# Optimization experiments

Measured on AMD Instinct MI355X. Metric: run time of the kernel, lower is better.

Reference implementation:

```python
import jax, jax.numpy as jnp
import numpy as np

B, N, NPOINT, K = 16, 4096, 1024, 8
CIN, COUT = 128, 256
RADIUS = 0.2
BN_EPS = 1e-5


def fps(pts, npoint):
    # pts: [B, N, 3] -> indices [B, npoint], farthest point sampling starting at index 0
    b, n, _ = pts.shape

    def body(carry, _):
        dists, last = carry  # dists [B,N], last [B]
        cur = jnp.take_along_axis(pts, last[:, None, None], axis=1)  # [B,1,3]
        d = jnp.sum((pts - cur) ** 2, axis=-1)  # [B,N]
        dists = jnp.minimum(dists, d)
        nxt = jnp.argmax(dists, axis=-1).astype(jnp.int32)
        return (dists, nxt), last

    init = (jnp.full((b, n), jnp.finfo(pts.dtype).max, pts.dtype),
            jnp.zeros((b,), jnp.int32))
    _, idxs = jax.lax.scan(body, init, None, length=npoint)  # [npoint, B]
    return idxs.T  # [B, npoint]


def ball_query(new_xyz, pts, radius, k):
    # new_xyz [B,S,3], pts [B,N,3] -> idx [B,S,k] (pad with first in-ball index, pointnet2 semantics)
    n = pts.shape[1]
    d2 = jnp.sum((new_xyz[:, :, None, :] - pts[:, None, :, :]) ** 2, axis=-1)  # [B,S,N]
    cand = jnp.where(d2 <= radius * radius, jnp.arange(n, dtype=jnp.int32), n)
    idx = jnp.sort(cand, axis=-1)[..., :k]  # first k in-ball indices (center always in-ball)
    idx = jnp.where(idx == n, idx[..., :1], idx)
    return idx


def setup_inputs() -> dict:
    key = jax.random.key(0)
    ks = jax.random.split(key, 8)
    xyz = jax.random.uniform(ks[0], (B, 3, N), dtype=jnp.float32)
    feat = jax.random.normal(ks[1], (B, CIN, N), dtype=jnp.float32)
    conv_w = jax.random.normal(ks[2], (COUT, CIN), dtype=jnp.float32) * (1.0 / np.sqrt(CIN))
    conv_b = jax.random.normal(ks[3], (COUT,), dtype=jnp.float32) * 0.01
    bn_gamma = jax.random.uniform(ks[4], (COUT,), dtype=jnp.float32, minval=0.5, maxval=1.5)
    bn_beta = jax.random.normal(ks[5], (COUT,), dtype=jnp.float32) * 0.1
    bn_mean = jax.random.normal(ks[6], (COUT,), dtype=jnp.float32) * 0.1
    bn_var = jax.random.uniform(ks[7], (COUT,), dtype=jnp.float32, minval=0.5, maxval=1.5)
    return {"xyz": xyz, "feat": feat, "conv_w": conv_w, "conv_b": conv_b,
            "bn_gamma": bn_gamma, "bn_beta": bn_beta, "bn_mean": bn_mean, "bn_var": bn_var}


def reference(xyz, feat, conv_w, conv_b, bn_gamma, bn_beta, bn_mean, bn_var):
    pts = jnp.transpose(xyz, (0, 2, 1))   # [B,N,3]
    fts = jnp.transpose(feat, (0, 2, 1))  # [B,N,F]

    fps_idx = fps(pts, NPOINT)                                        # [B,S]
    new_xyz = jnp.take_along_axis(pts, fps_idx[..., None], axis=1)    # [B,S,3]

    idx = ball_query(new_xyz, pts, RADIUS, K)                          # [B,S,K]
    grouped = jax.vmap(lambda f, i: f[i])(fts, idx)                    # [B,S,K,F]

    # shared pointwise Conv1d (kernel 1) + BatchNorm (inference stats) + ReLU
    x = jnp.einsum('bskf,of->bsko', grouped, conv_w) + conv_b          # [B,S,K,COUT]
    x = bn_gamma * (x - bn_mean) / jnp.sqrt(bn_var + BN_EPS) + bn_beta
    x = jax.nn.relu(x)
    new_feat = jnp.max(x, axis=2)                                      # [B,S,COUT]
    return new_xyz, new_feat
```

## Files before the change

### kernel.cpp

```cpp
#include <hip/hip_runtime.h>
#include <hip/hip_bf16.h>
#include <stdint.h>

#define Bn   16
#define Nn   4096
#define Sn   1024
#define Kn   8
#define CINn 128
#define COUTn 256

typedef __attribute__((ext_vector_type(8))) short bf16x8;
typedef __attribute__((ext_vector_type(4))) float f32x4;
typedef unsigned short ushort;
typedef __attribute__((ext_vector_type(8))) unsigned short ushort8;

static __device__ __forceinline__ float sqdist(float ax, float ay, float az,
                                               float bx, float by, float bz) {
    float dx = __fsub_rn(ax, bx);
    float dy = __fsub_rn(ay, by);
    float dz = __fsub_rn(az, bz);
    return __fadd_rn(__fadd_rn(__fmul_rn(dx, dx), __fmul_rn(dy, dy)), __fmul_rn(dz, dz));
}

static __device__ __forceinline__ unsigned long long u64max(unsigned long long a,
                                                            unsigned long long b) {
    return a > b ? a : b;
}

static __device__ __forceinline__ ushort f2bf(float f) {
    unsigned x = __float_as_uint(f);
    unsigned r = x + 0x7FFFu + ((x >> 16) & 1u);
    return (ushort)(r >> 16);
}

template <int CTRL>
static __device__ __forceinline__ void dpp_max_level(int& lo, int& hi) {
    int olo = __builtin_amdgcn_update_dpp(lo, lo, CTRL, 0xF, 0xF, false);
    int ohi = __builtin_amdgcn_update_dpp(hi, hi, CTRL, 0xF, 0xF, false);
    unsigned long long o = ((unsigned long long)(unsigned)ohi << 32) | (unsigned)olo;
    unsigned long long k = ((unsigned long long)(unsigned)hi << 32) | (unsigned)lo;
    if (o > k) { lo = olo; hi = ohi; }
}

static __device__ __forceinline__ unsigned long long wave_max_u64(unsigned long long key) {
    int lo = (int)(unsigned)(key & 0xFFFFFFFFull);
    int hi = (int)(unsigned)(key >> 32);
    dpp_max_level<0x111>(lo, hi);
    dpp_max_level<0x112>(lo, hi);
    dpp_max_level<0x114>(lo, hi);
    dpp_max_level<0x118>(lo, hi);
    dpp_max_level<0x142>(lo, hi);
    dpp_max_level<0x143>(lo, hi);
    unsigned flo = (unsigned)__builtin_amdgcn_readlane(lo, 63);
    unsigned fhi = (unsigned)__builtin_amdgcn_readlane(hi, 63);
    return ((unsigned long long)fhi << 32) | flo;
}

__global__ __launch_bounds__(256) void k_fps(const float* __restrict__ xyz,
                                             float* __restrict__ out_xyz) {
    __shared__ __align__(16) float xs[Nn], ys[Nn], zs[Nn];
    __shared__ __align__(16) unsigned long long gbuf[2][4];
    const int b = blockIdx.x;
    const int tid = threadIdx.x;
    const int wid = tid >> 6, lane = tid & 63;
    const float* base = xyz + (size_t)b * 3 * Nn;
    for (int i = tid; i < Nn; i += 256) {
        xs[i] = base[i];
        ys[i] = base[Nn + i];
        zs[i] = base[2 * Nn + i];
    }
    __syncthreads();
    float px[16], py[16], pz[16], dist[16];
#pragma unroll
    for (int j = 0; j < 16; ++j) {
        int p = tid + j * 256;
        px[j] = xs[p]; py[j] = ys[p]; pz[j] = zs[p];
        dist[j] = 3.402823466e+38f;
    }
    int last = 0;
    if (tid == 0) {
        out_xyz[(size_t)(b * Sn) * 3 + 0] = xs[0];
        out_xyz[(size_t)(b * Sn) * 3 + 1] = ys[0];
        out_xyz[(size_t)(b * Sn) * 3 + 2] = zs[0];
    }
    for (int s = 1; s < Sn; ++s) {
        const float cx = xs[last], cy = ys[last], cz = zs[last];
        float mv = -1.0f; int mi = 0;
#pragma unroll
        for (int j = 0; j < 16; ++j) {
            float d = sqdist(px[j], py[j], pz[j], cx, cy, cz);
            float nd = fminf(dist[j], d);
            dist[j] = nd;
            if (nd > mv) { mv = nd; mi = tid + j * 256; }
        }
        unsigned long long key =
            ((unsigned long long)__float_as_uint(mv) << 32) | (unsigned)(Nn - 1 - mi);
        key = wave_max_u64(key);
        if (lane == 0) gbuf[s & 1][wid] = key;
        __syncthreads();
        const ulonglong2 g0 = *(const ulonglong2*)&gbuf[s & 1][0];
        const ulonglong2 g1 = *(const ulonglong2*)&gbuf[s & 1][2];
        key = u64max(u64max(g0.x, g0.y), u64max(g1.x, g1.y));
        const int nl = Nn - 1 - (int)(unsigned)(key & 0xFFFFFFFFull);
        if (tid == 0) {
            out_xyz[(size_t)(b * Sn + s) * 3 + 0] = xs[nl];
            out_xyz[(size_t)(b * Sn + s) * 3 + 1] = ys[nl];
            out_xyz[(size_t)(b * Sn + s) * 3 + 2] = zs[nl];
        }
        last = nl;
    }
}

static __device__ __forceinline__ void wave_ball(const float* __restrict__ base,
                                                 float cx, float cy, float cz,
                                                 int lane, int* bslot) {
    int cnt = 0;
    int idx0 = -1;
    for (int chunk = 0; chunk < Nn / 64; ++chunk) {
        const int p = chunk * 64 + lane;
        const float d2 = sqdist(base[p], base[Nn + p], base[2 * Nn + p], cx, cy, cz);
        const bool in = (d2 <= 0.04f);
        const unsigned long long m = __ballot(in);
        if (m != 0ull) {
            if (idx0 < 0) idx0 = chunk * 64 + __builtin_ctzll(m);
            const int rank = cnt + __popcll(m & ((1ull << lane) - 1ull));
            if (in && rank < Kn)
                bslot[rank] = p;
            cnt += __popcll(m);
            if (cnt >= Kn) break;
        }
    }
    if (lane < Kn && lane >= cnt)
        bslot[lane] = idx0;
}

__global__ __launch_bounds__(512) void k_feat(const float* __restrict__ xyz,
                                              const float* __restrict__ out_xyz,
                                              const float* __restrict__ feat,
                                              const float* __restrict__ conv_w,
                                              const float* __restrict__ conv_b,
                                              const float* __restrict__ bn_g,
                                              const float* __restrict__ bn_b,
                                              const float* __restrict__ bn_m,
                                              const float* __restrict__ bn_v,
                                              float* __restrict__ out_feat) {
    __shared__ __align__(16) ushort A_lds[64][136];
    __shared__ __align__(16) ushort Wc[COUTn][40];
    __shared__ int bidx[8][Kn];
    const int tid = threadIdx.x;
    const int wave = tid >> 6, lane = tid & 63;
    const int b  = blockIdx.x & 15;
    const int c0 = (blockIdx.x >> 4) * 8;
    const int bs = b * Sn + c0 + wave;

    const float* base = xyz + (size_t)b * 3 * Nn;
    const float cx = out_xyz[(size_t)bs * 3 + 0];
    const float cy = out_xyz[(size_t)bs * 3 + 1];
    const float cz = out_xyz[(size_t)bs * 3 + 2];
    wave_ball(base, cx, cy, cz, lane, &bidx[wave][0]);
    __syncthreads();

    const float* fb = feat + (size_t)b * CINn * Nn;
    {
        const int r = tid >> 3, fo = tid & 7;
        const int pt = bidx[r >> 3][r & 7];
        ushort us[16];
#pragma unroll
        for (int i = 0; i < 16; ++i)
            us[i] = f2bf(fb[(size_t)(fo * 16 + i) * Nn + pt]);
        *(ushort8*)&A_lds[r][fo * 16]     = *(const ushort8*)&us[0];
        *(ushort8*)&A_lds[r][fo * 16 + 8] = *(const ushort8*)&us[8];
    }

    const int wo = tid >> 1, wfh = tid & 1;
    float4 stgW[4];
    {
        const float4* src = (const float4*)(conv_w + (size_t)wo * CINn + wfh * 16);
#pragma unroll
        for (int i = 0; i < 4; ++i) stgW[i] = src[i];
    }

    const int mt = wave & 3;
    const int obase = (wave >> 2) * 128;
    f32x4 acc[8];
#pragma unroll
    for (int t = 0; t < 8; ++t) acc[t] = (f32x4){0.f, 0.f, 0.f, 0.f};

    const int arow = mt * 16 + (lane & 15);
    const int kgrp = (lane >> 4) * 8;

#pragma unroll
    for (int ks = 0; ks < 4; ++ks) {
        {
            ushort us[16];
#pragma unroll
            for (int i = 0; i < 4; ++i) {
                us[i * 4 + 0] = f2bf(stgW[i].x);
                us[i * 4 + 1] = f2bf(stgW[i].y);
                us[i * 4 + 2] = f2bf(stgW[i].z);
                us[i * 4 + 3] = f2bf(stgW[i].w);
            }
            *(ushort8*)&Wc[wo][wfh * 16]     = *(const ushort8*)&us[0];
            *(ushort8*)&Wc[wo][wfh * 16 + 8] = *(const ushort8*)&us[8];
        }
        __syncthreads();
        if (ks < 3) {
            const float4* src = (const float4*)(conv_w + (size_t)wo * CINn +
                                                (ks + 1) * 32 + wfh * 16);
#pragma unroll
            for (int i = 0; i < 4; ++i) stgW[i] = src[i];
        }
        const bf16x8 a = *(const bf16x8*)&A_lds[arow][ks * 32 + kgrp];
#pragma unroll
        for (int t = 0; t < 8; ++t) {
            const int o = obase + t * 16 + (lane & 15);
            const bf16x8 bb = *(const bf16x8*)&Wc[o][kgrp];
            acc[t] = __builtin_amdgcn_mfma_f32_16x16x32_bf16(a, bb, acc[t], 0, 0, 0);
        }
        __syncthreads();
    }

    const int half = lane >> 4;
#pragma unroll
    for (int t = 0; t < 8; ++t) {
        const int o = obase + t * 16 + (lane & 15);
        const float bias = conv_b[o];
        const float g = bn_g[o], be = bn_b[o], mn = bn_m[o], vr = bn_v[o];
        const float inv = sqrtf(vr + 1e-5f);
        float m4 = -3.402823466e+38f;
#pragma unroll
        for (int i = 0; i < 4; ++i) {
            float z = acc[t][i] + bias;
            float y = g * (z - mn) / inv + be;
            y = fmaxf(y, 0.0f);
            m4 = fmaxf(m4, y);
        }
        const float mo = __shfl_xor(m4, 16);
        const float mx = fmaxf(m4, mo);
        if (half == 0)
            out_feat[(size_t)(b * Sn + c0 + mt * 2) * COUTn + o] = mx;
        else if (half == 2)
            out_feat[(size_t)(b * Sn + c0 + mt * 2 + 1) * COUTn + o] = mx;
    }
}

extern "C" void kernel_launch(void* const* d_in, const int* in_sizes, int n_in,
                              void* d_out, int out_size, void* d_ws, size_t ws_size,
                              hipStream_t stream) {
    const float* xyz    = (const float*)d_in[0];
    const float* feat   = (const float*)d_in[1];
    const float* conv_w = (const float*)d_in[2];
    const float* conv_b = (const float*)d_in[3];
    const float* bn_g   = (const float*)d_in[4];
    const float* bn_b   = (const float*)d_in[5];
    const float* bn_m   = (const float*)d_in[6];
    const float* bn_v   = (const float*)d_in[7];

    float* out_xyz  = (float*)d_out;
    float* out_feat = out_xyz + (size_t)Bn * Sn * 3;

    k_fps <<<dim3(Bn),           dim3(256), 0, stream>>>(xyz, out_xyz);
    k_feat<<<dim3(Bn * Sn / 8),  dim3(512), 0, stream>>>(xyz, out_xyz, feat,
                                                         conv_w, conv_b,
                                                         bn_g, bn_b, bn_m, bn_v,
                                                         out_feat);
}
```

Baseline: 707.3 us.

## Pack FPS distance math into float2 and broadcast winner coords via shared memory

The FPS loop now uses two-wide float vectors so the compiler can emit packed FP32 ops (v_pk_*) for the distance update. The winning lane of each wave writes the candidate point's coordinates next to its key, so after the barrier every thread selects the new centroid coordinates directly. This removes the dependent LDS lookup of xs/ys/zs by index at the start of each iteration. Each thread now does a speculative LDS read of its local argmax coordinates every step, and fp contract is disabled to keep rounding identical.

```diff
diff --git a/kernel.cpp b/kernel.cpp
--- a/kernel.cpp
+++ b/kernel.cpp
@@ -11,6 +11,7 @@
 
 typedef __attribute__((ext_vector_type(8))) short bf16x8;
 typedef __attribute__((ext_vector_type(4))) float f32x4;
+typedef __attribute__((ext_vector_type(2))) float f32x2;
 typedef unsigned short ushort;
 typedef __attribute__((ext_vector_type(8))) unsigned short ushort8;
 
@@ -58,11 +59,13 @@
 
 __global__ __launch_bounds__(256) void k_fps(const float* __restrict__ xyz,
                                              float* __restrict__ out_xyz) {
+#pragma clang fp contract(off)
     __shared__ __align__(16) float xs[Nn], ys[Nn], zs[Nn];
-    __shared__ __align__(16) unsigned long long gbuf[2][4];
+    __shared__ __align__(16) unsigned long long kbuf[2][4];
+    __shared__ __align__(16) float4 cbuf[2][4];
     const int b = blockIdx.x;
     const int tid = threadIdx.x;
-    const int wid = tid >> 6, lane = tid & 63;
+    const int wid = tid >> 6;
     const float* base = xyz + (size_t)b * 3 * Nn;
     for (int i = tid; i < Nn; i += 256) {
         xs[i] = base[i];
@@ -70,44 +73,67 @@
         zs[i] = base[2 * Nn + i];
     }
     __syncthreads();
-    float px[16], py[16], pz[16], dist[16];
-#pragma unroll
-    for (int j = 0; j < 16; ++j) {
-        int p = tid + j * 256;
-        px[j] = xs[p]; py[j] = ys[p]; pz[j] = zs[p];
-        dist[j] = 3.402823466e+38f;
-    }
-    int last = 0;
+    f32x2 px[8], py[8], pz[8], dist[8];
+#pragma unroll
+    for (int j = 0; j < 8; ++j) {
+        const int p0 = tid + (2 * j) * 256, p1 = p0 + 256;
+        px[j] = (f32x2){xs[p0], xs[p1]};
+        py[j] = (f32x2){ys[p0], ys[p1]};
+        pz[j] = (f32x2){zs[p0], zs[p1]};
+        dist[j] = (f32x2){3.402823466e+38f, 3.402823466e+38f};
+    }
+    float cx = xs[0], cy = ys[0], cz = zs[0];
     if (tid == 0) {
-        out_xyz[(size_t)(b * Sn) * 3 + 0] = xs[0];
-        out_xyz[(size_t)(b * Sn) * 3 + 1] = ys[0];
-        out_xyz[(size_t)(b * Sn) * 3 + 2] = zs[0];
+        out_xyz[(size_t)(b * Sn) * 3 + 0] = cx;
+        out_xyz[(size_t)(b * Sn) * 3 + 1] = cy;
+        out_xyz[(size_t)(b * Sn) * 3 + 2] = cz;
     }
     for (int s = 1; s < Sn; ++s) {
-        const float cx = xs[last], cy = ys[last], cz = zs[last];
+        const f32x2 cx2 = (f32x2){cx, cx};
+        const f32x2 cy2 = (f32x2){cy, cy};
+        const f32x2 cz2 = (f32x2){cz, cz};
         float mv = -1.0f; int mi = 0;
 #pragma unroll
-        for (int j = 0; j < 16; ++j) {
-            float d = sqdist(px[j], py[j], pz[j], cx, cy, cz);
-            float nd = fminf(dist[j], d);
-            dist[j] = nd;
-            if (nd > mv) { mv = nd; mi = tid + j * 256; }
-        }
-        unsigned long long key =
+        for (int j = 0; j < 8; ++j) {
+            f32x2 dx = px[j] - cx2;
+            f32x2 dy = py[j] - cy2;
+            f32x2 dz = pz[j] - cz2;
+            f32x2 xx = dx * dx, yy = dy * dy, zz = dz * dz;
+            f32x2 ss = (xx + yy) + zz;
+            const float n0 = fminf(dist[j].x, ss.x);
+            const float n1 = fminf(dist[j].y, ss.y);
+            dist[j].x = n0; dist[j].y = n1;
+            if (n0 > mv) { mv = n0; mi = tid + (2 * j) * 256; }
+            if (n1 > mv) { mv = n1; mi = tid + (2 * j + 1) * 256; }
+        }
+        const float wx = xs[mi], wy = ys[mi], wz = zs[mi];
+        const unsigned long long mykey =
             ((unsigned long long)__float_as_uint(mv) << 32) | (unsigned)(Nn - 1 - mi);
-        key = wave_max_u64(key);
-        if (lane == 0) gbuf[s & 1][wid] = key;
+        const unsigned long long wkey = wave_max_u64(mykey);
+        if (mykey == wkey) {
+            kbuf[s & 1][wid] = wkey;
+            cbuf[s & 1][wid] = make_float4(wx, wy, wz, 0.0f);
+        }
         __syncthreads();
-        const ulonglong2 g0 = *(const ulonglong2*)&gbuf[s & 1][0];
-        const ulonglong2 g1 = *(const ulonglong2*)&gbuf[s & 1][2];
-        key = u64max(u64max(g0.x, g0.y), u64max(g1.x, g1.y));
-        const int nl = Nn - 1 - (int)(unsigned)(key & 0xFFFFFFFFull);
+        const ulonglong2 kv0 = *(const ulonglong2*)&kbuf[s & 1][0];
+        const ulonglong2 kv1 = *(const ulonglong2*)&kbuf[s & 1][2];
+        const float4 c0 = cbuf[s & 1][0];
+        const float4 c1 = cbuf[s & 1][1];
+        const float4 c2 = cbuf[s & 1][2];
+        const float4 c3 = cbuf[s & 1][3];
+        const bool b01 = kv0.y > kv0.x;
+        const bool b23 = kv1.y > kv1.x;
+        const unsigned long long k01 = b01 ? kv0.y : kv0.x;
+        const unsigned long long k23 = b23 ? kv1.y : kv1.x;
+        const float4 ca = b01 ? c1 : c0;
+        const float4 cb = b23 ? c3 : c2;
+        const float4 cw = (k23 > k01) ? cb : ca;
+        cx = cw.x; cy = cw.y; cz = cw.z;
         if (tid == 0) {
-            out_xyz[(size_t)(b * Sn + s) * 3 + 0] = xs[nl];
-            out_xyz[(size_t)(b * Sn + s) * 3 + 1] = ys[nl];
-            out_xyz[(size_t)(b * Sn + s) * 3 + 2] = zs[nl];
-        }
-        last = nl;
+            out_xyz[(size_t)(b * Sn + s) * 3 + 0] = cx;
+            out_xyz[(size_t)(b * Sn + s) * 3 + 1] = cy;
+            out_xyz[(size_t)(b * Sn + s) * 3 + 2] = cz;
+        }
     }
 }
 
```

Result: no change. 709.4 us (+0.3%).

## Fuse FPS and grouping/conv into one persistent kernel with progress flags

Applied to the files above, without the earlier changes.

Merges the FPS kernel and the ball-query/conv kernel into a single persistent launch. 16 blocks run FPS and publish a per-batch progress counter every 64 samples. The remaining blocks spin on that counter and process feature tiles as soon as their centroids are ready. This overlaps the serial FPS phase with the grouping and MFMA work, which previously ran only after FPS finished. The cost is a spin-wait protocol built on relaxed atomics, and the whole scheme relies on all 240 blocks being co-resident on the GPU.

```diff
diff --git a/kernel.cpp b/kernel.cpp
--- a/kernel.cpp
+++ b/kernel.cpp
@@ -9,10 +9,18 @@
 #define CINn 128
 #define COUTn 256
 
+#define NFPS 16
+#define NBLK 240
+
 typedef __attribute__((ext_vector_type(8))) short bf16x8;
 typedef __attribute__((ext_vector_type(4))) float f32x4;
 typedef unsigned short ushort;
 typedef __attribute__((ext_vector_type(8))) unsigned short ushort8;
+
+#define ATOM_ST_F32(p, v) __hip_atomic_store((p), (v), __ATOMIC_RELAXED, __HIP_MEMORY_SCOPE_AGENT)
+#define ATOM_LD_F32(p)    __hip_atomic_load((p), __ATOMIC_RELAXED, __HIP_MEMORY_SCOPE_AGENT)
+#define ATOM_ST_I32(p, v) __hip_atomic_store((p), (v), __ATOMIC_RELAXED, __HIP_MEMORY_SCOPE_AGENT)
+#define ATOM_LD_I32(p)    __hip_atomic_load((p), __ATOMIC_RELAXED, __HIP_MEMORY_SCOPE_AGENT)
 
 static __device__ __forceinline__ float sqdist(float ax, float ay, float az,
                                                float bx, float by, float bz) {
@@ -54,61 +62,6 @@
     unsigned flo = (unsigned)__builtin_amdgcn_readlane(lo, 63);
     unsigned fhi = (unsigned)__builtin_amdgcn_readlane(hi, 63);
     return ((unsigned long long)fhi << 32) | flo;
-}
-
-__global__ __launch_bounds__(256) void k_fps(const float* __restrict__ xyz,
-                                             float* __restrict__ out_xyz) {
-    __shared__ __align__(16) float xs[Nn], ys[Nn], zs[Nn];
-    __shared__ __align__(16) unsigned long long gbuf[2][4];
-    const int b = blockIdx.x;
-    const int tid = threadIdx.x;
-    const int wid = tid >> 6, lane = tid & 63;
-    const float* base = xyz + (size_t)b * 3 * Nn;
-    for (int i = tid; i < Nn; i += 256) {
-        xs[i] = base[i];
-        ys[i] = base[Nn + i];
-        zs[i] = base[2 * Nn + i];
-    }
-    __syncthreads();
-    float px[16], py[16], pz[16], dist[16];
-#pragma unroll
-    for (int j = 0; j < 16; ++j) {
-        int p = tid + j * 256;
-        px[j] = xs[p]; py[j] = ys[p]; pz[j] = zs[p];
-        dist[j] = 3.402823466e+38f;
-    }
-    int last = 0;
-    if (tid == 0) {
-        out_xyz[(size_t)(b * Sn) * 3 + 0] = xs[0];
-        out_xyz[(size_t)(b * Sn) * 3 + 1] = ys[0];
-        out_xyz[(size_t)(b * Sn) * 3 + 2] = zs[0];
-    }
-    for (int s = 1; s < Sn; ++s) {
-        const float cx = xs[last], cy = ys[last], cz = zs[last];
-        float mv = -1.0f; int mi = 0;
-#pragma unroll
-        for (int j = 0; j < 16; ++j) {
-            float d = sqdist(px[j], py[j], pz[j], cx, cy, cz);
-            float nd = fminf(dist[j], d);
-            dist[j] = nd;
-            if (nd > mv) { mv = nd; mi = tid + j * 256; }
-        }
-        unsigned long long key =
-            ((unsigned long long)__float_as_uint(mv) << 32) | (unsigned)(Nn - 1 - mi);
-        key = wave_max_u64(key);
-        if (lane == 0) gbuf[s & 1][wid] = key;
-        __syncthreads();
-        const ulonglong2 g0 = *(const ulonglong2*)&gbuf[s & 1][0];
-        const ulonglong2 g1 = *(const ulonglong2*)&gbuf[s & 1][2];
-        key = u64max(u64max(g0.x, g0.y), u64max(g1.x, g1.y));
-        const int nl = Nn - 1 - (int)(unsigned)(key & 0xFFFFFFFFull);
-        if (tid == 0) {
-            out_xyz[(size_t)(b * Sn + s) * 3 + 0] = xs[nl];
-            out_xyz[(size_t)(b * Sn + s) * 3 + 1] = ys[nl];
-            out_xyz[(size_t)(b * Sn + s) * 3 + 2] = zs[nl];
-        }
-        last = nl;
-    }
 }
 
 static __device__ __forceinline__ void wave_ball(const float* __restrict__ base,
@@ -134,113 +87,194 @@
         bslot[lane] = idx0;
 }
 
-__global__ __launch_bounds__(512) void k_feat(const float* __restrict__ xyz,
-                                              const float* __restrict__ out_xyz,
-                                              const float* __restrict__ feat,
-                                              const float* __restrict__ conv_w,
-                                              const float* __restrict__ conv_b,
-                                              const float* __restrict__ bn_g,
-                                              const float* __restrict__ bn_b,
-                                              const float* __restrict__ bn_m,
-                                              const float* __restrict__ bn_v,
-                                              float* __restrict__ out_feat) {
-    __shared__ __align__(16) ushort A_lds[64][136];
-    __shared__ __align__(16) ushort Wc[COUTn][40];
-    __shared__ int bidx[8][Kn];
+__global__ __launch_bounds__(512, 2) void k_fused(
+        const float* __restrict__ xyz,
+        const float* __restrict__ feat,
+        const float* __restrict__ conv_w,
+        const float* __restrict__ conv_b,
+        const float* __restrict__ bn_g,
+        const float* __restrict__ bn_b,
+        const float* __restrict__ bn_m,
+        const float* __restrict__ bn_v,
+        float* __restrict__ out_xyz,
+        float* __restrict__ out_feat,
+        int* __restrict__ progress) {
+    __shared__ __align__(16) char shm[86016];
     const int tid = threadIdx.x;
+    const int bid = blockIdx.x;
+
+    if (bid < NFPS) {
+        const int b = bid;
+        if (tid >= 256) {
+            for (int s = 0; s < Sn; ++s) __syncthreads();
+            return;
+        }
+        float* xs = (float*)shm;
+        float* ys = xs + Nn;
+        float* zs = ys + Nn;
+        unsigned long long (*gbuf)[4] =
+            (unsigned long long(*)[4])(shm + 3 * Nn * sizeof(float));
+        const int wid = tid >> 6, lane = tid & 63;
+        const float* base = xyz + (size_t)b * 3 * Nn;
+        for (int i = tid; i < Nn; i += 256) {
+            xs[i] = base[i];
+            ys[i] = base[Nn + i];
+            zs[i] = base[2 * Nn + i];
+        }
+        __syncthreads();
+        float px[16], py[16], pz[16], dist[16];
+#pragma unroll
+        for (int j = 0; j < 16; ++j) {
+            int p = tid + j * 256;
+            px[j] = xs[p]; py[j] = ys[p]; pz[j] = zs[p];
+            dist[j] = 3.402823466e+38f;
+        }
+        int last = 0;
+        if (tid == 0) {
+            ATOM_ST_F32(&out_xyz[(size_t)(b * Sn) * 3 + 0], xs[0]);
+            ATOM_ST_F32(&out_xyz[(size_t)(b * Sn) * 3 + 1], ys[0]);
+            ATOM_ST_F32(&out_xyz[(size_t)(b * Sn) * 3 + 2], zs[0]);
+        }
+        for (int s = 1; s < Sn; ++s) {
+            const float cx = xs[last], cy = ys[last], cz = zs[last];
+            float mv = -1.0f; int mi = 0;
+#pragma unroll
+            for (int j = 0; j < 16; ++j) {
+                float d = sqdist(px[j], py[j], pz[j], cx, cy, cz);
+                float nd = fminf(dist[j], d);
+                dist[j] = nd;
+                if (nd > mv) { mv = nd; mi = tid + j * 256; }
+            }
+            unsigned long long key =
+                ((unsigned long long)__float_as_uint(mv) << 32) |
+                (unsigned)(Nn - 1 - mi);
+            key = wave_max_u64(key);
+            if (lane == 0) gbuf[s & 1][wid] = key;
+            __syncthreads();
+            const ulonglong2 g0 = *(const ulonglong2*)&gbuf[s & 1][0];
+            const ulonglong2 g1 = *(const ulonglong2*)&gbuf[s & 1][2];
+            key = u64max(u64max(g0.x, g0.y), u64max(g1.x, g1.y));
+            const int nl = Nn - 1 - (int)(unsigned)(key & 0xFFFFFFFFull);
+            if (tid == 0) {
+                ATOM_ST_F32(&out_xyz[(size_t)(b * Sn + s) * 3 + 0], xs[nl]);
+                ATOM_ST_F32(&out_xyz[(size_t)(b * Sn + s) * 3 + 1], ys[nl]);
+                ATOM_ST_F32(&out_xyz[(size_t)(b * Sn + s) * 3 + 2], zs[nl]);
+                if ((s & 63) == 63) {
+                    asm volatile("s_waitcnt vmcnt(0)" ::: "memory");
+                    ATOM_ST_I32(progress + b, s + 1);
+                }
+            }
+            last = nl;
+        }
+        return;
+    }
+
+    ushort (*A_lds)[136] = (ushort(*)[136])shm;
+    ushort (*Wc)[40]     = (ushort(*)[40])(shm + 17408);
+    int (*bidx)[Kn]      = (int(*)[Kn])(shm + 17408 + 20480);
     const int wave = tid >> 6, lane = tid & 63;
-    const int b  = blockIdx.x & 15;
-    const int c0 = (blockIdx.x >> 4) * 8;
-    const int bs = b * Sn + c0 + wave;
-
-    const float* base = xyz + (size_t)b * 3 * Nn;
-    const float cx = out_xyz[(size_t)bs * 3 + 0];
-    const float cy = out_xyz[(size_t)bs * 3 + 1];
-    const float cz = out_xyz[(size_t)bs * 3 + 2];
-    wave_ball(base, cx, cy, cz, lane, &bidx[wave][0]);
-    __syncthreads();
-
-    const float* fb = feat + (size_t)b * CINn * Nn;
-    {
-        const int r = tid >> 3, fo = tid & 7;
-        const int pt = bidx[r >> 3][r & 7];
-        ushort us[16];
-#pragma unroll
-        for (int i = 0; i < 16; ++i)
-            us[i] = f2bf(fb[(size_t)(fo * 16 + i) * Nn + pt]);
-        *(ushort8*)&A_lds[r][fo * 16]     = *(const ushort8*)&us[0];
-        *(ushort8*)&A_lds[r][fo * 16 + 8] = *(const ushort8*)&us[8];
-    }
-
-    const int wo = tid >> 1, wfh = tid & 1;
-    float4 stgW[4];
-    {
-        const float4* src = (const float4*)(conv_w + (size_t)wo * CINn + wfh * 16);
-#pragma unroll
-        for (int i = 0; i < 4; ++i) stgW[i] = src[i];
-    }
-
-    const int mt = wave & 3;
-    const int obase = (wave >> 2) * 128;
-    f32x4 acc[8];
-#pragma unroll
-    for (int t = 0; t < 8; ++t) acc[t] = (f32x4){0.f, 0.f, 0.f, 0.f};
-
-    const int arow = mt * 16 + (lane & 15);
-    const int kgrp = (lane >> 4) * 8;
-
-#pragma unroll
-    for (int ks = 0; ks < 4; ++ks) {
+
+    for (int t = bid - NFPS; t < Bn * Sn / 8; t += NBLK - NFPS) {
+        const int b  = t & 15;
+        const int c0 = (t >> 4) * 8;
+        const int bs = b * Sn + c0 + wave;
+
+        if (tid == 0) {
+            while (ATOM_LD_I32(progress + b) < c0 + 8)
+                __builtin_amdgcn_s_sleep(8);
+        }
+        __syncthreads();
+
+        const float cx = ATOM_LD_F32(&out_xyz[(size_t)bs * 3 + 0]);
+        const float cy = ATOM_LD_F32(&out_xyz[(size_t)bs * 3 + 1]);
+        const float cz = ATOM_LD_F32(&out_xyz[(size_t)bs * 3 + 2]);
+
+        const float* base = xyz + (size_t)b * 3 * Nn;
+        wave_ball(base, cx, cy, cz, lane, &bidx[wave][0]);
+        __syncthreads();
+
+        const float* fb = feat + (size_t)b * CINn * Nn;
         {
+            const int r = tid >> 3, fo = tid & 7;
+            const int pt = bidx[r >> 3][r & 7];
             ushort us[16];
 #pragma unroll
+            for (int i = 0; i < 16; ++i)
+                us[i] = f2bf(fb[(size_t)(fo * 16 + i) * Nn + pt]);
+            *(ushort8*)&A_lds[r][fo * 16]     = *(const ushort8*)&us[0];
+            *(ushort8*)&A_lds[r][fo * 16 + 8] = *(const ushort8*)&us[8];
+        }
+
+        const int wo = tid >> 1, wfh = tid & 1;
+        float4 stgW[4];
+        {
+            const float4* src = (const float4*)(conv_w + (size_t)wo * CINn + wfh * 16);
+#pragma unroll
+            for (int i = 0; i < 4; ++i) stgW[i] = src[i];
+        }
+
+        const int mt = wave & 3;
+        const int obase = (wave >> 2) * 128;
+        f32x4 acc[8];
+#pragma unroll
+        for (int tt = 0; tt < 8; ++tt) acc[tt] = (f32x4){0.f, 0.f, 0.f, 0.f};
+
+        const int arow = mt * 16 + (lane & 15);
+        const int kgrp = (lane >> 4) * 8;
+
+#pragma unroll
+        for (int ks = 0; ks < 4; ++ks) {
+            {
+                ushort us[16];
+#pragma unroll
+                for (int i = 0; i < 4; ++i) {
+                    us[i * 4 + 0] = f2bf(stgW[i].x);
+                    us[i * 4 + 1] = f2bf(stgW[i].y);
+                    us[i * 4 + 2] = f2bf(stgW[i].z);
+                    us[i * 4 + 3] = f2bf(stgW[i].w);
+                }
+                *(ushort8*)&Wc[wo][wfh * 16]     = *(const ushort8*)&us[0];
+                *(ushort8*)&Wc[wo][wfh * 16 + 8] = *(const ushort8*)&us[8];
+            }
+            __syncthreads();
+            if (ks < 3) {
+                const float4* src = (const float4*)(conv_w + (size_t)wo * CINn +
+                                                    (ks + 1) * 32 + wfh * 16);
+#pragma unroll
+                for (int i = 0; i < 4; ++i) stgW[i] = src[i];
+            }
+            const bf16x8 a = *(const bf16x8*)&A_lds[arow][ks * 32 + kgrp];
+#pragma unroll
+            for (int tt = 0; tt < 8; ++tt) {
+                const int o = obase + tt * 16 + (lane & 15);
+                const bf16x8 bb = *(const bf16x8*)&Wc[o][kgrp];
+                acc[tt] = __builtin_amdgcn_mfma_f32_16x16x32_bf16(a, bb, acc[tt], 0, 0, 0);
+            }
+            __syncthreads();
+        }
+
+        const int half = lane >> 4;
+#pragma unroll
+        for (int tt = 0; tt < 8; ++tt) {
+            const int o = obase + tt * 16 + (lane & 15);
+            const float bias = conv_b[o];
+            const float g = bn_g[o], be = bn_b[o], mn = bn_m[o], vr = bn_v[o];
+            const float inv = sqrtf(vr + 1e-5f);
+            float m4 = -3.402823466e+38f;
+#pragma unroll
             for (int i = 0; i < 4; ++i) {
-                us[i * 4 + 0] = f2bf(stgW[i].x);
-                us[i * 4 + 1] = f2bf(stgW[i].y);
-                us[i * 4 + 2] = f2bf(stgW[i].z);
-                us[i * 4 + 3] = f2bf(stgW[i].w);
-            }
-            *(ushort8*)&Wc[wo][wfh * 16]     = *(const ushort8*)&us[0];
-            *(ushort8*)&Wc[wo][wfh * 16 + 8] = *(const ushort8*)&us[8];
-        }
-        __syncthreads();
-        if (ks < 3) {
-            const float4* src = (const float4*)(conv_w + (size_t)wo * CINn +
-                                                (ks + 1) * 32 + wfh * 16);
-#pragma unroll
-            for (int i = 0; i < 4; ++i) stgW[i] = src[i];
-        }
-        const bf16x8 a = *(const bf16x8*)&A_lds[arow][ks * 32 + kgrp];
-#pragma unroll
-        for (int t = 0; t < 8; ++t) {
-            const int o = obase + t * 16 + (lane & 15);
-            const bf16x8 bb = *(const bf16x8*)&Wc[o][kgrp];
-            acc[t] = __builtin_amdgcn_mfma_f32_16x16x32_bf16(a, bb, acc[t], 0, 0, 0);
-        }
-        __syncthreads();
-    }
-
-    const int half = lane >> 4;
-#pragma unroll
-    for (int t = 0; t < 8; ++t) {
-        const int o = obase + t * 16 + (lane & 15);
-        const float bias = conv_b[o];
-        const float g = bn_g[o], be = bn_b[o], mn = bn_m[o], vr = bn_v[o];
-        const float inv = sqrtf(vr + 1e-5f);
-        float m4 = -3.402823466e+38f;
-#pragma unroll
-        for (int i = 0; i < 4; ++i) {
-            float z = acc[t][i] + bias;
-            float y = g * (z - mn) / inv + be;
-            y = fmaxf(y, 0.0f);
-            m4 = fmaxf(m4, y);
-        }
-        const float mo = __shfl_xor(m4, 16);
-        const float mx = fmaxf(m4, mo);
-        if (half == 0)
-            out_feat[(size_t)(b * Sn + c0 + mt * 2) * COUTn + o] = mx;
-        else if (half == 2)
-            out_feat[(size_t)(b * Sn + c0 + mt * 2 + 1) * COUTn + o] = mx;
+                float z = acc[tt][i] + bias;
+                float y = g * (z - mn) / inv + be;
+                y = fmaxf(y, 0.0f);
+                m4 = fmaxf(m4, y);
+            }
+            const float mo = __shfl_xor(m4, 16);
+            const float mx = fmaxf(m4, mo);
+            if (half == 0)
+                out_feat[(size_t)(b * Sn + c0 + mt * 2) * COUTn + o] = mx;
+            else if (half == 2)
+                out_feat[(size_t)(b * Sn + c0 + mt * 2 + 1) * COUTn + o] = mx;
+        }
     }
 }
 
@@ -259,9 +293,10 @@
     float* out_xyz  = (float*)d_out;
     float* out_feat = out_xyz + (size_t)Bn * Sn * 3;
 
-    k_fps <<<dim3(Bn),           dim3(256), 0, stream>>>(xyz, out_xyz);
-    k_feat<<<dim3(Bn * Sn / 8),  dim3(512), 0, stream>>>(xyz, out_xyz, feat,
-                                                         conv_w, conv_b,
-                                                         bn_g, bn_b, bn_m, bn_v,
-                                                         out_feat);
-}
+    int* progress = (int*)d_ws;
+    hipMemsetAsync(progress, 0, Bn * sizeof(int), stream);
+
+    k_fused<<<dim3(NBLK), dim3(512), 0, stream>>>(xyz, feat, conv_w, conv_b,
+                                                  bn_g, bn_b, bn_m, bn_v,
+                                                  out_xyz, out_feat, progress);
+}
```

After: 692.3 us (median of 2 runs). -2.1%, faster.
